# Kernel tuning notes

Measured on AMD Instinct MI355X. Metric: run time of the kernel, lower is better.

The kernel has to match this reference:

```python
import jax, jax.numpy as jnp
import numpy as np

SRC_LEN, TGT_LEN, BATCH = 256, 128, 256
NH, NE, NSYM = 512, 256, 64


def setup_inputs() -> dict:
    key = jax.random.key(0)
    ks = jax.random.split(key, 14)
    w = lambda k, shape: jax.random.normal(k, shape, jnp.float32) * 0.05
    return {
        "src_enc": jax.random.normal(ks[0], (SRC_LEN, BATCH, NH), jnp.float32),
        "tgt": jax.random.randint(ks[1], (TGT_LEN, BATCH, 1), 0, NSYM, jnp.int32),
        "src_lengths": jax.random.randint(ks[2], (BATCH,), 1, SRC_LEN + 1, jnp.int32),
        "emb_table": w(ks[3], (NSYM, NE)),
        "Ws_w": w(ks[4], (NH, NH)), "Ws_b": jnp.zeros((NH,), jnp.float32),
        "Wz_w": w(ks[5], (NH, NE + 2 * NH)), "Wz_b": jnp.zeros((NH,), jnp.float32),
        "Wr_w": w(ks[6], (NH, NE + 2 * NH)), "Wr_b": jnp.zeros((NH,), jnp.float32),
        "Wn_w": w(ks[7], (NH, NE + 2 * NH)), "Wn_b": jnp.zeros((NH,), jnp.float32),
        "Wa_w": w(ks[8], (NH, 2 * NH)), "Wa_b": jnp.zeros((NH,), jnp.float32),
        "va_w": w(ks[9], (1, NH)),
        "Wo_w": w(ks[10], (NH, NE + 2 * NH)), "Wo_b": jnp.zeros((NH,), jnp.float32),
    }


def reference(src_enc, tgt, src_lengths, emb_table,
              Ws_w, Ws_b, Wz_w, Wz_b, Wr_w, Wr_b, Wn_w, Wn_b,
              Wa_w, Wa_b, va_w, Wo_w, Wo_b):
    src_len, batch, nh = src_enc.shape
    # src_mask: [src_len, batch] True where position < length
    mask = jnp.arange(src_len)[:, None] < src_lengths[None, :]
    tgt_embed = emb_table[tgt[..., 0]]                     # [T, B, E]
    s0 = jnp.tanh(src_enc[0] @ Ws_w.T + Ws_b)              # [B, H]
    # Split Wa into the s-part and src_enc-part; encoder projection is
    # loop-invariant, compute it once (same math as cat+Linear).
    Wa_s, Wa_e = Wa_w[:, :nh], Wa_w[:, nh:]
    enc_proj = jnp.einsum('sbh,gh->sbg', src_enc, Wa_e) + Wa_b  # [S, B, H]
    va = va_w[0]                                           # [H]
    neg_inf = jnp.float32(-jnp.inf)

    def step(s, emb_i):
        h = jnp.tanh(enc_proj + s @ Wa_s.T)                # [S, B, H]
        ei = jnp.einsum('sbh,h->sb', h, va)                # [S, B]
        ei = jnp.where(mask, ei, neg_inf)
        ai = jax.nn.softmax(ei, axis=0)                    # [S, B]
        ci = jnp.einsum('sb,sbh->bh', ai, src_enc)         # [B, H]
        x = jnp.concatenate([emb_i, s, ci], axis=-1)       # [B, E+2H]
        ti = x @ Wo_w.T + Wo_b
        zi = jax.nn.sigmoid(x @ Wz_w.T + Wz_b)
        ri = jax.nn.sigmoid(x @ Wr_w.T + Wr_b)
        xn = jnp.concatenate([emb_i, ri * s, ci], axis=-1)
        ni = jnp.tanh(xn @ Wn_w.T + Wn_b)
        s_new = (1.0 - zi) * s + zi * ni
        return s_new, (ti, s, ai.T)

    _, (dec_outputs, dec_states, dec_attns) = jax.lax.scan(step, s0, tgt_embed[:-1])
    # dec_outputs/dec_states: [T-1, B, H]; dec_attns: [T-1, B, S]
    return dec_outputs, dec_states, dec_attns
```

## Files before the change

kernel.cpp:

```cpp
#include <hip/hip_runtime.h>
#include <hip/hip_bf16.h>
#include <cstdint>
#include <cstddef>

namespace {

constexpr int S_LEN  = 256;
constexpr int BATCH  = 256;
constexpr int NH     = 512;
constexpr int NE     = 256;
constexpr int NSTEPS = 127;
constexpr int KX     = NE + 2*NH;
constexpr int N1     = 3*NH;
constexpr size_t SB        = (size_t)S_LEN * BATCH;
constexpr size_t SRC_ELEMS = SB * NH;

typedef __attribute__((ext_vector_type(8))) short  short8v;
typedef __attribute__((ext_vector_type(4))) float  float4v;

__device__ __forceinline__ float bf2f(unsigned short u) {
  union { unsigned int i; float f; } c; c.i = ((unsigned int)u) << 16; return c.f;
}
__device__ __forceinline__ unsigned short f2bf(float f) {
  union { float f; unsigned int i; } c; c.f = f;
  unsigned int x = c.i;
  return (unsigned short)((x + 0x7FFFu + ((x >> 16) & 1u)) >> 16);
}
__device__ __forceinline__ float fast_tanh(float x) {
  float ax = __builtin_fabsf(x);
  float e  = __expf(-2.f * ax);
  float r  = (1.f - e) * __builtin_amdgcn_rcpf(1.f + e);
  return x < 0.f ? -r : r;
}
__device__ __forceinline__ float fast_sigmoid(float x) {
  return __builtin_amdgcn_rcpf(1.f + __expf(-x));
}


__global__ void k_conv_src(const float* __restrict__ src, unsigned short* __restrict__ dst) {
  size_t i = (size_t)blockIdx.x * blockDim.x + threadIdx.x;
  size_t stride = (size_t)gridDim.x * blockDim.x;
  for (size_t j = i * 4; j < SRC_ELEMS; j += stride * 4) {
    float4 v = *(const float4*)(src + j);
    dst[j+0] = f2bf(v.x); dst[j+1] = f2bf(v.y);
    dst[j+2] = f2bf(v.z); dst[j+3] = f2bf(v.w);
  }
}

__global__ void k_conv_w(const float* __restrict__ Wo, const float* __restrict__ Wz,
                         const float* __restrict__ Wr, const float* __restrict__ Wn,
                         const float* __restrict__ Wa,
                         const float* __restrict__ Wob, const float* __restrict__ Wzb,
                         const float* __restrict__ Wrb,
                         unsigned short* __restrict__ W1, unsigned short* __restrict__ WnB,
                         unsigned short* __restrict__ Was, unsigned short* __restrict__ Wae,
                         float* __restrict__ b1) {
  const int TOT_W1 = N1 * KX;
  const int TOT_WN = NH * KX;
  const int TOT_WA = NH * NH;
  const int total  = TOT_W1 + TOT_WN + 2*TOT_WA + N1;
  int i = blockIdx.x * blockDim.x + threadIdx.x;
  int stride = gridDim.x * blockDim.x;
  for (; i < total; i += stride) {
    int idx = i;
    if (idx < TOT_W1) {
      int row = idx / KX, col = idx % KX;
      float v = (row < NH) ? Wo[row*KX+col]
              : (row < 2*NH) ? Wz[(row-NH)*KX+col]
                             : Wr[(row-2*NH)*KX+col];
      W1[idx] = f2bf(v);
    } else if ((idx -= TOT_W1) < TOT_WN) {
      WnB[idx] = f2bf(Wn[idx]);
    } else if ((idx -= TOT_WN) < TOT_WA) {
      int g = idx / NH, j = idx % NH;
      Was[idx] = f2bf(Wa[g*(2*NH) + j]);
    } else if ((idx -= TOT_WA) < TOT_WA) {
      int g = idx / NH, h = idx % NH;
      Wae[idx] = f2bf(Wa[g*(2*NH) + NH + h]);
    } else {
      idx -= TOT_WA;
      b1[idx] = (idx < NH) ? Wob[idx] : (idx < 2*NH) ? Wzb[idx-NH] : Wrb[idx-2*NH];
    }
  }
}

__global__ void k_emb(const int* __restrict__ tgt, const float* __restrict__ table,
                      unsigned short* __restrict__ emb) {
  const int total = NSTEPS * BATCH * NE;
  int i = blockIdx.x * blockDim.x + threadIdx.x;
  int stride = gridDim.x * blockDim.x;
  for (; i < total; i += stride) {
    int e  = i & (NE - 1);
    int tb = i >> 8;
    int sym = tgt[tb];
    emb[i] = f2bf(table[sym * NE + e]);
  }
}

__global__ __launch_bounds__(256) void k_s0(
    const float* __restrict__ src, const float* __restrict__ Wsw,
    const float* __restrict__ Wsb, const unsigned short* __restrict__ emb0,
    float* __restrict__ s_f32, unsigned short* __restrict__ x) {
  __shared__ float sv[NH];
  const int b = blockIdx.x, tid = threadIdx.x;
  sv[tid]       = src[(size_t)b*NH + tid];
  sv[tid + 256] = src[(size_t)b*NH + tid + 256];
  __syncthreads();
  for (int j = tid; j < NH; j += 256) {
    float acc = Wsb[j];
    const float* wr = Wsw + (size_t)j*NH;
    #pragma unroll 8
    for (int h = 0; h < NH; h++) acc += sv[h] * wr[h];
    float s = fast_tanh(acc);
    s_f32[b*NH + j]     = s;
    x[b*KX + NE + j]    = f2bf(s);
  }
  if (tid < NE) x[b*KX + tid] = emb0[b*NE + tid];
}

template<bool OUT_BF16, bool HAS_BIAS>
__global__ __launch_bounds__(256) void k_gemm(
    const unsigned short* __restrict__ A, int lda,
    const unsigned short* __restrict__ B, int ldb,
    void* __restrict__ C, int ldc,
    const float* __restrict__ bias, int K) {
  __shared__ alignas(16) unsigned short As[64][32];
  __shared__ alignas(16) unsigned short Bs[64][32];
  const int tid  = threadIdx.x;
  const int m0   = blockIdx.x * 64, n0 = blockIdx.y * 64;
  const int lane = tid & 63, wave = tid >> 6;
  const int wm   = (wave >> 1) * 32, wn = (wave & 1) * 32;
  const int srow = tid >> 2, scol = (tid & 3) * 8;
  const int fr   = lane & 15, kq = lane >> 4;
  float4v acc00 = {0.f,0.f,0.f,0.f}, acc01 = {0.f,0.f,0.f,0.f};
  float4v acc10 = {0.f,0.f,0.f,0.f}, acc11 = {0.f,0.f,0.f,0.f};
  const unsigned short* Aptr = A + (size_t)(m0 + srow) * lda + scol;
  const unsigned short* Bptr = B + (size_t)(n0 + srow) * ldb + scol;
  for (int k0 = 0; k0 < K; k0 += 32) {
    *(short8v*)&As[srow][scol] = *(const short8v*)(Aptr + k0);
    *(short8v*)&Bs[srow][scol] = *(const short8v*)(Bptr + k0);
    __syncthreads();
    short8v a0 = *(const short8v*)&As[wm + fr][kq*8];
    short8v a1 = *(const short8v*)&As[wm + 16 + fr][kq*8];
    short8v b0 = *(const short8v*)&Bs[wn + fr][kq*8];
    short8v b1 = *(const short8v*)&Bs[wn + 16 + fr][kq*8];
    acc00 = __builtin_amdgcn_mfma_f32_16x16x32_bf16(a0, b0, acc00, 0, 0, 0);
    acc01 = __builtin_amdgcn_mfma_f32_16x16x32_bf16(a0, b1, acc01, 0, 0, 0);
    acc10 = __builtin_amdgcn_mfma_f32_16x16x32_bf16(a1, b0, acc10, 0, 0, 0);
    acc11 = __builtin_amdgcn_mfma_f32_16x16x32_bf16(a1, b1, acc11, 0, 0, 0);
    __syncthreads();
  }
  const int rq = lane >> 4;
  #pragma unroll
  for (int am = 0; am < 2; am++) {
    float4v accb0 = am ? acc10 : acc00;
    float4v accb1 = am ? acc11 : acc01;
    #pragma unroll
    for (int r = 0; r < 4; r++) {
      int row = m0 + wm + am*16 + rq*4 + r;
      int c0  = n0 + wn + fr;
      int c1  = n0 + wn + 16 + fr;
      float v0 = accb0[r], v1 = accb1[r];
      if (HAS_BIAS) { v0 += bias[c0]; v1 += bias[c1]; }
      if (OUT_BF16) {
        ((unsigned short*)C)[(size_t)row*ldc + c0] = f2bf(v0);
        ((unsigned short*)C)[(size_t)row*ldc + c1] = f2bf(v1);
      } else {
        ((float*)C)[(size_t)row*ldc + c0] = v0;
        ((float*)C)[(size_t)row*ldc + c1] = v1;
      }
    }
  }
}

__global__ __launch_bounds__(512) void k_attn(
    const unsigned short* __restrict__ ep,
    const unsigned short* __restrict__ srcb,
    const float* __restrict__ sWa,
    const float* __restrict__ va,
    const int* __restrict__ slen,
    float* __restrict__ attn_out,
    unsigned short* __restrict__ x) {
  __shared__ float q[NH];
  __shared__ float vas[NH];
  __shared__ float ei[S_LEN];
  __shared__ float ai[S_LEN];
  __shared__ float red[8];
  const int b = blockIdx.x, tid = threadIdx.x;
  const int lane = tid & 63, wave = tid >> 6;
  q[tid]   = sWa[b*NH + tid];
  vas[tid] = va[tid];
  __syncthreads();
  const int len = slen[b];

  for (int s = wave; s < S_LEN; s += 8) {
    const unsigned short* p = ep + ((size_t)s*BATCH + b)*NH + lane*8;
    short8v v = *(const short8v*)p;
    float acc = 0.f;
    const int g0 = lane*8;
    #pragma unroll
    for (int j = 0; j < 8; j++) {
      float hv = fast_tanh(bf2f((unsigned short)v[j]) + q[g0+j]);
      acc += hv * vas[g0+j];
    }
    #pragma unroll
    for (int off = 32; off > 0; off >>= 1) acc += __shfl_xor(acc, off, 64);
    if (lane == 0) ei[s] = (s < len) ? acc : -3.0e38f;
  }
  __syncthreads();

  float e = (tid < S_LEN) ? ei[tid] : -3.0e38f;
  float m = e;
  #pragma unroll
  for (int off = 32; off > 0; off >>= 1) m = fmaxf(m, __shfl_xor(m, off, 64));
  if (lane == 0) red[wave] = m;
  __syncthreads();
  m = red[0];
  #pragma unroll
  for (int w = 1; w < 8; w++) m = fmaxf(m, red[w]);
  float p = (tid < S_LEN) ? __expf(e - m) : 0.f;
  float sum = p;
  #pragma unroll
  for (int off = 32; off > 0; off >>= 1) sum += __shfl_xor(sum, off, 64);
  __syncthreads();
  if (lane == 0) red[wave] = sum;
  __syncthreads();
  float tot = red[0];
  #pragma unroll
  for (int w = 1; w < 8; w++) tot += red[w];
  float inv = __builtin_amdgcn_rcpf(tot);
  if (tid < S_LEN) {
    float a = p * inv;
    ai[tid] = a;
    attn_out[(size_t)b*S_LEN + tid] = a;
  }
  __syncthreads();

  float acc = 0.f;
  const unsigned short* sp = srcb + (size_t)b*NH + tid;
  #pragma unroll 8
  for (int s = 0; s < S_LEN; s++) acc += ai[s] * bf2f(sp[(size_t)s * BATCH * NH]);
  x[b*KX + NE + NH + tid] = f2bf(acc);
}

__global__ __launch_bounds__(512) void k_mid(
    const float* __restrict__ Y, const float* __restrict__ s_f32,
    float* __restrict__ dec_out_t, float* __restrict__ zi,
    unsigned short* __restrict__ x) {
  const int b = blockIdx.x, tid = threadIdx.x;
  dec_out_t[(size_t)b*NH + tid] = Y[(size_t)b*N1 + tid];
  zi[b*NH + tid] = fast_sigmoid(Y[(size_t)b*N1 + NH + tid]);
  float r = fast_sigmoid(Y[(size_t)b*N1 + 2*NH + tid]);
  x[b*KX + NE + tid] = f2bf(r * s_f32[b*NH + tid]);
}

__global__ __launch_bounds__(512) void k_final(
    const float* __restrict__ npre, const float* __restrict__ zi,
    float* __restrict__ s_f32, float* __restrict__ dec_states_t,
    unsigned short* __restrict__ x, const unsigned short* __restrict__ emb_next,
    int has_next) {
  const int b = blockIdx.x, tid = threadIdx.x;
  float n  = fast_tanh(npre[b*NH + tid]);
  float z  = zi[b*NH + tid];
  float so = s_f32[b*NH + tid];
  float sn = (1.f - z)*so + z*n;
  dec_states_t[(size_t)b*NH + tid] = so;
  s_f32[b*NH + tid]  = sn;
  x[b*KX + NE + tid] = f2bf(sn);
  if (has_next && tid < NE) x[b*KX + tid] = emb_next[b*NE + tid];
}

}

extern "C" void kernel_launch(void* const* d_in, const int* in_sizes, int n_in,
                              void* d_out, int out_size, void* d_ws, size_t ws_size,
                              hipStream_t stream) {
  const float* src_enc  = (const float*)d_in[0];
  const int*   tgt      = (const int*)d_in[1];
  const int*   slen     = (const int*)d_in[2];
  const float* emb_tab  = (const float*)d_in[3];
  const float* Wsw      = (const float*)d_in[4];
  const float* Wsb      = (const float*)d_in[5];
  const float* Wzw      = (const float*)d_in[6];
  const float* Wzb      = (const float*)d_in[7];
  const float* Wrw      = (const float*)d_in[8];
  const float* Wrb      = (const float*)d_in[9];
  const float* Wnw      = (const float*)d_in[10];
  const float* Wnb      = (const float*)d_in[11];
  const float* Waw      = (const float*)d_in[12];
  const float* Wab      = (const float*)d_in[13];
  const float* vaw      = (const float*)d_in[14];
  const float* Wow      = (const float*)d_in[15];
  const float* Wob      = (const float*)d_in[16];

  char* ws = (char*)d_ws;
  size_t off = 0;
  auto alloc = [&](size_t bytes) -> void* {
    void* p = ws + off;
    off = (off + bytes + 255) & ~(size_t)255;
    return p;
  };
  unsigned short* src_bf = (unsigned short*)alloc(SRC_ELEMS * 2);
  unsigned short* ep     = (unsigned short*)alloc(SRC_ELEMS * 2);
  unsigned short* emb_bf = (unsigned short*)alloc((size_t)NSTEPS*BATCH*NE*2);
  unsigned short* W1     = (unsigned short*)alloc((size_t)N1*KX*2);
  unsigned short* WnB    = (unsigned short*)alloc((size_t)NH*KX*2);
  unsigned short* Was    = (unsigned short*)alloc((size_t)NH*NH*2);
  unsigned short* Wae    = (unsigned short*)alloc((size_t)NH*NH*2);
  float*          b1     = (float*)alloc((size_t)N1*4);
  unsigned short* x      = (unsigned short*)alloc((size_t)BATCH*KX*2);
  float*          s_f32  = (float*)alloc((size_t)BATCH*NH*4);
  float*          sWa    = (float*)alloc((size_t)BATCH*NH*4);
  float*          Y      = (float*)alloc((size_t)BATCH*N1*4);
  float*          zi     = (float*)alloc((size_t)BATCH*NH*4);
  float*          npre   = (float*)alloc((size_t)BATCH*NH*4);

  float* out         = (float*)d_out;
  float* dec_outputs = out;
  float* dec_states  = out + (size_t)NSTEPS*BATCH*NH;
  float* dec_attns   = dec_states + (size_t)NSTEPS*BATCH*NH;

  k_conv_src<<<4096, 256, 0, stream>>>(src_enc, src_bf);
  k_conv_w<<<2048, 256, 0, stream>>>(Wow, Wzw, Wrw, Wnw, Waw, Wob, Wzb, Wrb,
                                     W1, WnB, Was, Wae, b1);
  k_emb<<<2048, 256, 0, stream>>>(tgt, emb_tab, emb_bf);
  k_s0<<<BATCH, 256, 0, stream>>>(src_enc, Wsw, Wsb, emb_bf, s_f32, x);
  k_gemm<true, true><<<dim3(SB/64, NH/64), 256, 0, stream>>>(
      src_bf, NH, Wae, NH, ep, NH, Wab, NH);

  for (int t = 0; t < NSTEPS; t++) {
    k_gemm<false, false><<<dim3(BATCH/64, NH/64), 256, 0, stream>>>(
        x + NE, KX, Was, NH, sWa, NH, nullptr, NH);
    k_attn<<<BATCH, 512, 0, stream>>>(ep, src_bf, sWa, vaw, slen,
                                      dec_attns + (size_t)t*BATCH*S_LEN, x);
    k_gemm<false, true><<<dim3(BATCH/64, N1/64), 256, 0, stream>>>(
        x, KX, W1, KX, Y, N1, b1, KX);
    k_mid<<<BATCH, 512, 0, stream>>>(Y, s_f32, dec_outputs + (size_t)t*BATCH*NH, zi, x);
    k_gemm<false, true><<<dim3(BATCH/64, NH/64), 256, 0, stream>>>(
        x, KX, WnB, KX, npre, NH, Wnb, KX);
    k_final<<<BATCH, 512, 0, stream>>>(npre, zi, s_f32,
                                       dec_states + (size_t)t*BATCH*NH, x,
                                       emb_bf + (size_t)(t+1)*BATCH*NE,
                                       (t+1) < NSTEPS ? 1 : 0);
  }
}
```

Before: 11.83 ms.

## Fuse GRU gate elementwise ops into GEMM epilogues and split Wn by input part

Splits the Wn projection so the emb and ci terms are computed together with the Wo/Wz/Wr GEMM (N=2048), and only the r*s part needs a second small K=512 GEMM. The k_mid and k_final elementwise kernels are folded into GEMM epilogues, and the concatenated x buffer is replaced by separate pointers read directly by the GEMM. The GEMM moves to 64-wide K tiles with double-buffered, XOR-swizzled LDS, and the s0 projection now uses the MFMA GEMM. This cuts launches and intermediate traffic per step and shrinks the Wn GEMM's K, at the cost of branchy epilogues and more A-load pointer logic.

```diff
diff --git a/kernel.cpp b/kernel.cpp
--- a/kernel.cpp
+++ b/kernel.cpp
@@ -10,34 +10,33 @@
 constexpr int NH     = 512;
 constexpr int NE     = 256;
 constexpr int NSTEPS = 127;
-constexpr int KX     = NE + 2*NH;
-constexpr int N1     = 3*NH;
+constexpr int N1     = 2048;
 constexpr size_t SB        = (size_t)S_LEN * BATCH;
 constexpr size_t SRC_ELEMS = SB * NH;
 
 typedef __attribute__((ext_vector_type(8))) short  short8v;
 typedef __attribute__((ext_vector_type(4))) float  float4v;
-
-__device__ __forceinline__ float bf2f(unsigned short u) {
+typedef unsigned short us;
+
+constexpr int EPI_F32 = 0, EPI_EPROJ = 1, EPI_STEP1 = 2, EPI_STEP2 = 3, EPI_S0 = 4;
+
+__device__ __forceinline__ float bf2f(us u) {
   union { unsigned int i; float f; } c; c.i = ((unsigned int)u) << 16; return c.f;
 }
-__device__ __forceinline__ unsigned short f2bf(float f) {
+__device__ __forceinline__ us f2bf(float f) {
   union { float f; unsigned int i; } c; c.f = f;
   unsigned int x = c.i;
-  return (unsigned short)((x + 0x7FFFu + ((x >> 16) & 1u)) >> 16);
-}
-__device__ __forceinline__ float fast_tanh(float x) {
-  float ax = __builtin_fabsf(x);
-  float e  = __expf(-2.f * ax);
-  float r  = (1.f - e) * __builtin_amdgcn_rcpf(1.f + e);
-  return x < 0.f ? -r : r;
-}
-__device__ __forceinline__ float fast_sigmoid(float x) {
+  return (us)((x + 0x7FFFu + ((x >> 16) & 1u)) >> 16);
+}
+__device__ __forceinline__ float tanh2(float x) {
+  return 1.f - 2.f * __builtin_amdgcn_rcpf(__expf(2.f * x) + 1.f);
+}
+__device__ __forceinline__ float sigm(float x) {
   return __builtin_amdgcn_rcpf(1.f + __expf(-x));
 }
 
 
-__global__ void k_conv_src(const float* __restrict__ src, unsigned short* __restrict__ dst) {
+__global__ void k_conv_src(const float* __restrict__ src, us* __restrict__ dst) {
   size_t i = (size_t)blockIdx.x * blockDim.x + threadIdx.x;
   size_t stride = (size_t)gridDim.x * blockDim.x;
   for (size_t j = i * 4; j < SRC_ELEMS; j += stride * 4) {
@@ -49,43 +48,53 @@
 
 __global__ void k_conv_w(const float* __restrict__ Wo, const float* __restrict__ Wz,
                          const float* __restrict__ Wr, const float* __restrict__ Wn,
-                         const float* __restrict__ Wa,
+                         const float* __restrict__ Wa, const float* __restrict__ Ws,
                          const float* __restrict__ Wob, const float* __restrict__ Wzb,
-                         const float* __restrict__ Wrb,
-                         unsigned short* __restrict__ W1, unsigned short* __restrict__ WnB,
-                         unsigned short* __restrict__ Was, unsigned short* __restrict__ Wae,
-                         float* __restrict__ b1) {
-  const int TOT_W1 = N1 * KX;
-  const int TOT_WN = NH * KX;
-  const int TOT_WA = NH * NH;
-  const int total  = TOT_W1 + TOT_WN + 2*TOT_WA + N1;
+                         const float* __restrict__ Wrb, const float* __restrict__ Wnb,
+                         us* __restrict__ W1cat, us* __restrict__ Wns,
+                         us* __restrict__ Was, us* __restrict__ Wae,
+                         us* __restrict__ Wsbf, float* __restrict__ bcat) {
+  const int T1 = 2048 * 1280;
+  const int T2 = 512 * 512;
+  const int total = T1 + 4 * T2 + 2048;
   int i = blockIdx.x * blockDim.x + threadIdx.x;
   int stride = gridDim.x * blockDim.x;
   for (; i < total; i += stride) {
     int idx = i;
-    if (idx < TOT_W1) {
-      int row = idx / KX, col = idx % KX;
-      float v = (row < NH) ? Wo[row*KX+col]
-              : (row < 2*NH) ? Wz[(row-NH)*KX+col]
-                             : Wr[(row-2*NH)*KX+col];
-      W1[idx] = f2bf(v);
-    } else if ((idx -= TOT_W1) < TOT_WN) {
-      WnB[idx] = f2bf(Wn[idx]);
-    } else if ((idx -= TOT_WN) < TOT_WA) {
-      int g = idx / NH, j = idx % NH;
-      Was[idx] = f2bf(Wa[g*(2*NH) + j]);
-    } else if ((idx -= TOT_WA) < TOT_WA) {
-      int g = idx / NH, h = idx % NH;
-      Wae[idx] = f2bf(Wa[g*(2*NH) + NH + h]);
+    if (idx < T1) {
+      int row = idx / 1280, col = idx - row * 1280;
+      float v;
+      if      (row < 512)  v = Wo[row * 1280 + col];
+      else if (row < 1024) v = Wz[(row - 512) * 1280 + col];
+      else if (row < 1536) v = Wr[(row - 1024) * 1280 + col];
+      else {
+        int g = row - 1536;
+        v = (col >= 256 && col < 768) ? 0.f : Wn[g * 1280 + col];
+      }
+      W1cat[idx] = f2bf(v);
+    } else if ((idx -= T1) < T2) {
+      int g = idx >> 9, j = idx & 511;
+      Wns[idx] = f2bf(Wn[g * 1280 + 256 + j]);
+    } else if ((idx -= T2) < T2) {
+      int g = idx >> 9, h = idx & 511;
+      Was[idx] = f2bf(Wa[g * 1024 + h]);
+    } else if ((idx -= T2) < T2) {
+      int g = idx >> 9, h = idx & 511;
+      Wae[idx] = f2bf(Wa[g * 1024 + 512 + h]);
+    } else if ((idx -= T2) < T2) {
+      Wsbf[idx] = f2bf(Ws[idx]);
     } else {
-      idx -= TOT_WA;
-      b1[idx] = (idx < NH) ? Wob[idx] : (idx < 2*NH) ? Wzb[idx-NH] : Wrb[idx-2*NH];
+      idx -= T2;
+      bcat[idx] = (idx < 512) ? Wob[idx]
+                : (idx < 1024) ? Wzb[idx - 512]
+                : (idx < 1536) ? Wrb[idx - 1024]
+                               : Wnb[idx - 1536];
     }
   }
 }
 
 __global__ void k_emb(const int* __restrict__ tgt, const float* __restrict__ table,
-                      unsigned short* __restrict__ emb) {
+                      us* __restrict__ emb) {
   const int total = NSTEPS * BATCH * NE;
   int i = blockIdx.x * blockDim.x + threadIdx.x;
   int stride = gridDim.x * blockDim.x;
@@ -97,112 +106,156 @@
   }
 }
 
-__global__ __launch_bounds__(256) void k_s0(
-    const float* __restrict__ src, const float* __restrict__ Wsw,
-    const float* __restrict__ Wsb, const unsigned short* __restrict__ emb0,
-    float* __restrict__ s_f32, unsigned short* __restrict__ x) {
-  __shared__ float sv[NH];
-  const int b = blockIdx.x, tid = threadIdx.x;
-  sv[tid]       = src[(size_t)b*NH + tid];
-  sv[tid + 256] = src[(size_t)b*NH + tid + 256];
-  __syncthreads();
-  for (int j = tid; j < NH; j += 256) {
-    float acc = Wsb[j];
-    const float* wr = Wsw + (size_t)j*NH;
-    #pragma unroll 8
-    for (int h = 0; h < NH; h++) acc += sv[h] * wr[h];
-    float s = fast_tanh(acc);
-    s_f32[b*NH + j]     = s;
-    x[b*KX + NE + j]    = f2bf(s);
-  }
-  if (tid < NE) x[b*KX + tid] = emb0[b*NE + tid];
-}
-
-template<bool OUT_BF16, bool HAS_BIAS>
-__global__ __launch_bounds__(256) void k_gemm(
-    const unsigned short* __restrict__ A, int lda,
-    const unsigned short* __restrict__ B, int ldb,
-    void* __restrict__ C, int ldc,
-    const float* __restrict__ bias, int K) {
-  __shared__ alignas(16) unsigned short As[64][32];
-  __shared__ alignas(16) unsigned short Bs[64][32];
-  const int tid  = threadIdx.x;
-  const int m0   = blockIdx.x * 64, n0 = blockIdx.y * 64;
+template<int EPI>
+__global__ __launch_bounds__(256) void k_g64(
+    const us* __restrict__ A0, const us* __restrict__ A1, const us* __restrict__ A2,
+    const us* __restrict__ Bw, int K,
+    const float* __restrict__ bias,
+    float* __restrict__ f0, float* __restrict__ f1, float* __restrict__ f2,
+    us* __restrict__ g0,
+    const float* __restrict__ sf) {
+  constexpr bool X3 = (EPI == EPI_STEP1);
+  __shared__ us As[2][4096];
+  __shared__ us Bs[2][4096];
+  const int tid = threadIdx.x;
+  const int m0 = blockIdx.x * 64, n0 = blockIdx.y * 64;
+  const int srow  = tid >> 2;
+  const int c0    = (tid & 3) * 16;
+  const int cbyte = c0 * 2;
+  const int nit   = K >> 6;
+  short8v ar0, ar1, br0, br1;
+
+  auto loadA = [&](int k0) {
+    const int cc0 = k0 + c0, cc1 = cc0 + 8;
+    if (X3) {
+      const us* p0 = (cc0 < 256) ? A0 + (size_t)(m0 + srow) * 256 + cc0
+                   : (cc0 < 768) ? A1 + (size_t)(m0 + srow) * 512 + (cc0 - 256)
+                                 : A2 + (size_t)(m0 + srow) * 512 + (cc0 - 768);
+      const us* p1 = (cc1 < 256) ? A0 + (size_t)(m0 + srow) * 256 + cc1
+                   : (cc1 < 768) ? A1 + (size_t)(m0 + srow) * 512 + (cc1 - 256)
+                                 : A2 + (size_t)(m0 + srow) * 512 + (cc1 - 768);
+      ar0 = *(const short8v*)p0;
+      ar1 = *(const short8v*)p1;
+    } else {
+      const us* p = A0 + (size_t)(m0 + srow) * K + cc0;
+      ar0 = *(const short8v*)p;
+      ar1 = *(const short8v*)(p + 8);
+    }
+    const us* q = Bw + (size_t)(n0 + srow) * K + cc0;
+    br0 = *(const short8v*)q;
+    br1 = *(const short8v*)(q + 8);
+  };
+  auto stage = [&](int buf) {
+    char* ab = (char*)As + buf * 8192;
+    char* bb = (char*)Bs + buf * 8192;
+    const int sw = (srow & 7) << 4;
+    const int o0 = srow * 128 + (cbyte ^ sw);
+    const int o1 = srow * 128 + ((cbyte + 16) ^ sw);
+    *(short8v*)(ab + o0) = ar0;
+    *(short8v*)(ab + o1) = ar1;
+    *(short8v*)(bb + o0) = br0;
+    *(short8v*)(bb + o1) = br1;
+  };
+
   const int lane = tid & 63, wave = tid >> 6;
-  const int wm   = (wave >> 1) * 32, wn = (wave & 1) * 32;
-  const int srow = tid >> 2, scol = (tid & 3) * 8;
-  const int fr   = lane & 15, kq = lane >> 4;
-  float4v acc00 = {0.f,0.f,0.f,0.f}, acc01 = {0.f,0.f,0.f,0.f};
-  float4v acc10 = {0.f,0.f,0.f,0.f}, acc11 = {0.f,0.f,0.f,0.f};
-  const unsigned short* Aptr = A + (size_t)(m0 + srow) * lda + scol;
-  const unsigned short* Bptr = B + (size_t)(n0 + srow) * ldb + scol;
-  for (int k0 = 0; k0 < K; k0 += 32) {
-    *(short8v*)&As[srow][scol] = *(const short8v*)(Aptr + k0);
-    *(short8v*)&Bs[srow][scol] = *(const short8v*)(Bptr + k0);
+  const int wm = (wave >> 1) * 32, wn = (wave & 1) * 32;
+  const int fr = lane & 15, kq = lane >> 4;
+  const int ra0 = wm + fr, ra1 = wm + 16 + fr;
+  const int rb0 = wn + fr, rb1 = wn + 16 + fr;
+  float4v acc00 = {0,0,0,0}, acc01 = {0,0,0,0}, acc10 = {0,0,0,0}, acc11 = {0,0,0,0};
+
+  loadA(0);
+  stage(0);
+  for (int it = 0; it < nit; ++it) {
     __syncthreads();
-    short8v a0 = *(const short8v*)&As[wm + fr][kq*8];
-    short8v a1 = *(const short8v*)&As[wm + 16 + fr][kq*8];
-    short8v b0 = *(const short8v*)&Bs[wn + fr][kq*8];
-    short8v b1 = *(const short8v*)&Bs[wn + 16 + fr][kq*8];
-    acc00 = __builtin_amdgcn_mfma_f32_16x16x32_bf16(a0, b0, acc00, 0, 0, 0);
-    acc01 = __builtin_amdgcn_mfma_f32_16x16x32_bf16(a0, b1, acc01, 0, 0, 0);
-    acc10 = __builtin_amdgcn_mfma_f32_16x16x32_bf16(a1, b0, acc10, 0, 0, 0);
-    acc11 = __builtin_amdgcn_mfma_f32_16x16x32_bf16(a1, b1, acc11, 0, 0, 0);
-    __syncthreads();
-  }
-  const int rq = lane >> 4;
-  #pragma unroll
-  for (int am = 0; am < 2; am++) {
-    float4v accb0 = am ? acc10 : acc00;
-    float4v accb1 = am ? acc11 : acc01;
-    #pragma unroll
-    for (int r = 0; r < 4; r++) {
-      int row = m0 + wm + am*16 + rq*4 + r;
-      int c0  = n0 + wn + fr;
-      int c1  = n0 + wn + 16 + fr;
-      float v0 = accb0[r], v1 = accb1[r];
-      if (HAS_BIAS) { v0 += bias[c0]; v1 += bias[c1]; }
-      if (OUT_BF16) {
-        ((unsigned short*)C)[(size_t)row*ldc + c0] = f2bf(v0);
-        ((unsigned short*)C)[(size_t)row*ldc + c1] = f2bf(v1);
-      } else {
-        ((float*)C)[(size_t)row*ldc + c0] = v0;
-        ((float*)C)[(size_t)row*ldc + c1] = v1;
+    if (it + 1 < nit) loadA((it + 1) << 6);
+    const char* ab = (const char*)As + (it & 1) * 8192;
+    const char* bb = (const char*)Bs + (it & 1) * 8192;
+    #pragma unroll
+    for (int ks = 0; ks < 2; ++ks) {
+      const int cb2 = ks * 64 + kq * 16;
+      short8v a0 = *(const short8v*)(ab + ra0 * 128 + (cb2 ^ ((ra0 & 7) << 4)));
+      short8v a1 = *(const short8v*)(ab + ra1 * 128 + (cb2 ^ ((ra1 & 7) << 4)));
+      short8v b0 = *(const short8v*)(bb + rb0 * 128 + (cb2 ^ ((rb0 & 7) << 4)));
+      short8v b1 = *(const short8v*)(bb + rb1 * 128 + (cb2 ^ ((rb1 & 7) << 4)));
+      acc00 = __builtin_amdgcn_mfma_f32_16x16x32_bf16(a0, b0, acc00, 0, 0, 0);
+      acc01 = __builtin_amdgcn_mfma_f32_16x16x32_bf16(a0, b1, acc01, 0, 0, 0);
+      acc10 = __builtin_amdgcn_mfma_f32_16x16x32_bf16(a1, b0, acc10, 0, 0, 0);
+      acc11 = __builtin_amdgcn_mfma_f32_16x16x32_bf16(a1, b1, acc11, 0, 0, 0);
+    }
+    if (it + 1 < nit) stage((it + 1) & 1);
+  }
+
+  #pragma unroll
+  for (int am = 0; am < 2; ++am) {
+    #pragma unroll
+    for (int bn = 0; bn < 2; ++bn) {
+      float4v a = am ? (bn ? acc11 : acc10) : (bn ? acc01 : acc00);
+      #pragma unroll
+      for (int r = 0; r < 4; ++r) {
+        const int rowO = m0 + wm + am * 16 + kq * 4 + r;
+        const int colO = n0 + wn + bn * 16 + fr;
+        float v = a[r];
+        if (EPI == EPI_F32) {
+          f0[(size_t)rowO * 512 + colO] = v;
+        } else if (EPI == EPI_S0) {
+          float tv = tanh2(v + bias[colO]);
+          f0[(size_t)rowO * 512 + colO] = tv;
+          g0[(size_t)rowO * 512 + colO] = f2bf(tv);
+        } else if (EPI == EPI_EPROJ) {
+          g0[(size_t)rowO * 512 + colO] = f2bf(v + bias[colO]);
+        } else if (EPI == EPI_STEP1) {
+          v += bias[colO];
+          const int q = colO >> 9, j = colO & 511;
+          const size_t idx = (size_t)rowO * 512 + j;
+          if      (q == 0) f0[idx] = v;
+          else if (q == 1) f1[idx] = sigm(v);
+          else if (q == 2) g0[idx] = f2bf(sigm(v) * sf[idx]);
+          else             f2[idx] = v;
+        } else {
+          const size_t idx = (size_t)rowO * 512 + colO;
+          float nv = tanh2(v + f2[idx]);
+          float z  = bias[idx];
+          float so = f1[idx];
+          float sn = (1.f - z) * so + z * nv;
+          f0[idx] = so;
+          f1[idx] = sn;
+          g0[idx] = f2bf(sn);
+        }
       }
     }
   }
 }
 
 __global__ __launch_bounds__(512) void k_attn(
-    const unsigned short* __restrict__ ep,
-    const unsigned short* __restrict__ srcb,
+    const us* __restrict__ ep,
+    const us* __restrict__ srcb,
     const float* __restrict__ sWa,
     const float* __restrict__ va,
     const int* __restrict__ slen,
     float* __restrict__ attn_out,
-    unsigned short* __restrict__ x) {
-  __shared__ float q[NH];
-  __shared__ float vas[NH];
+    us* __restrict__ ci_bf) {
   __shared__ float ei[S_LEN];
   __shared__ float ai[S_LEN];
   __shared__ float red[8];
   const int b = blockIdx.x, tid = threadIdx.x;
   const int lane = tid & 63, wave = tid >> 6;
-  q[tid]   = sWa[b*NH + tid];
-  vas[tid] = va[tid];
-  __syncthreads();
+  const int g0 = lane * 8;
+  float qv[8], vv[8];
+  {
+    const float* qp = sWa + b * NH + g0;
+    const float* vp = va + g0;
+    #pragma unroll
+    for (int j = 0; j < 8; j++) { qv[j] = qp[j]; vv[j] = vp[j]; }
+  }
   const int len = slen[b];
 
   for (int s = wave; s < S_LEN; s += 8) {
-    const unsigned short* p = ep + ((size_t)s*BATCH + b)*NH + lane*8;
-    short8v v = *(const short8v*)p;
+    short8v v = *(const short8v*)(ep + ((size_t)s * BATCH + b) * NH + g0);
     float acc = 0.f;
-    const int g0 = lane*8;
-    #pragma unroll
-    for (int j = 0; j < 8; j++) {
-      float hv = fast_tanh(bf2f((unsigned short)v[j]) + q[g0+j]);
-      acc += hv * vas[g0+j];
-    }
+    #pragma unroll
+    for (int j = 0; j < 8; j++)
+      acc += tanh2(bf2f((us)v[j]) + qv[j]) * vv[j];
     #pragma unroll
     for (int off = 32; off > 0; off >>= 1) acc += __shfl_xor(acc, off, 64);
     if (lane == 0) ei[s] = (s < len) ? acc : -3.0e38f;
@@ -232,42 +285,15 @@
   if (tid < S_LEN) {
     float a = p * inv;
     ai[tid] = a;
-    attn_out[(size_t)b*S_LEN + tid] = a;
+    attn_out[(size_t)b * S_LEN + tid] = a;
   }
   __syncthreads();
 
   float acc = 0.f;
-  const unsigned short* sp = srcb + (size_t)b*NH + tid;
+  const us* sp = srcb + (size_t)b * NH + tid;
   #pragma unroll 8
   for (int s = 0; s < S_LEN; s++) acc += ai[s] * bf2f(sp[(size_t)s * BATCH * NH]);
-  x[b*KX + NE + NH + tid] = f2bf(acc);
-}
-
-__global__ __launch_bounds__(512) void k_mid(
-    const float* __restrict__ Y, const float* __restrict__ s_f32,
-    float* __restrict__ dec_out_t, float* __restrict__ zi,
-    unsigned short* __restrict__ x) {
-  const int b = blockIdx.x, tid = threadIdx.x;
-  dec_out_t[(size_t)b*NH + tid] = Y[(size_t)b*N1 + tid];
-  zi[b*NH + tid] = fast_sigmoid(Y[(size_t)b*N1 + NH + tid]);
-  float r = fast_sigmoid(Y[(size_t)b*N1 + 2*NH + tid]);
-  x[b*KX + NE + tid] = f2bf(r * s_f32[b*NH + tid]);
-}
-
-__global__ __launch_bounds__(512) void k_final(
-    const float* __restrict__ npre, const float* __restrict__ zi,
-    float* __restrict__ s_f32, float* __restrict__ dec_states_t,
-    unsigned short* __restrict__ x, const unsigned short* __restrict__ emb_next,
-    int has_next) {
-  const int b = blockIdx.x, tid = threadIdx.x;
-  float n  = fast_tanh(npre[b*NH + tid]);
-  float z  = zi[b*NH + tid];
-  float so = s_f32[b*NH + tid];
-  float sn = (1.f - z)*so + z*n;
-  dec_states_t[(size_t)b*NH + tid] = so;
-  s_f32[b*NH + tid]  = sn;
-  x[b*KX + NE + tid] = f2bf(sn);
-  if (has_next && tid < NE) x[b*KX + tid] = emb_next[b*NE + tid];
+  ci_bf[b * NH + tid] = f2bf(acc);
 }
 
 }
@@ -300,47 +326,48 @@
     off = (off + bytes + 255) & ~(size_t)255;
     return p;
   };
-  unsigned short* src_bf = (unsigned short*)alloc(SRC_ELEMS * 2);
-  unsigned short* ep     = (unsigned short*)alloc(SRC_ELEMS * 2);
-  unsigned short* emb_bf = (unsigned short*)alloc((size_t)NSTEPS*BATCH*NE*2);
-  unsigned short* W1     = (unsigned short*)alloc((size_t)N1*KX*2);
-  unsigned short* WnB    = (unsigned short*)alloc((size_t)NH*KX*2);
-  unsigned short* Was    = (unsigned short*)alloc((size_t)NH*NH*2);
-  unsigned short* Wae    = (unsigned short*)alloc((size_t)NH*NH*2);
-  float*          b1     = (float*)alloc((size_t)N1*4);
-  unsigned short* x      = (unsigned short*)alloc((size_t)BATCH*KX*2);
-  float*          s_f32  = (float*)alloc((size_t)BATCH*NH*4);
-  float*          sWa    = (float*)alloc((size_t)BATCH*NH*4);
-  float*          Y      = (float*)alloc((size_t)BATCH*N1*4);
-  float*          zi     = (float*)alloc((size_t)BATCH*NH*4);
-  float*          npre   = (float*)alloc((size_t)BATCH*NH*4);
+  us*    src_bf = (us*)alloc(SRC_ELEMS * 2);
+  us*    ep     = (us*)alloc(SRC_ELEMS * 2);
+  us*    emb_bf = (us*)alloc((size_t)NSTEPS * BATCH * NE * 2);
+  us*    W1cat  = (us*)alloc((size_t)N1 * 1280 * 2);
+  us*    Wns    = (us*)alloc((size_t)512 * 512 * 2);
+  us*    Was    = (us*)alloc((size_t)512 * 512 * 2);
+  us*    Wae    = (us*)alloc((size_t)512 * 512 * 2);
+  us*    Wsbf   = (us*)alloc((size_t)512 * 512 * 2);
+  float* bcat   = (float*)alloc((size_t)N1 * 4);
+  float* s_f32  = (float*)alloc((size_t)BATCH * NH * 4);
+  us*    s_bf   = (us*)alloc((size_t)BATCH * NH * 2);
+  float* sWa    = (float*)alloc((size_t)BATCH * NH * 4);
+  float* zi     = (float*)alloc((size_t)BATCH * NH * 4);
+  float* npart  = (float*)alloc((size_t)BATCH * NH * 4);
+  us*    xn_bf  = (us*)alloc((size_t)BATCH * NH * 2);
+  us*    ci_bf  = (us*)alloc((size_t)BATCH * NH * 2);
 
   float* out         = (float*)d_out;
   float* dec_outputs = out;
-  float* dec_states  = out + (size_t)NSTEPS*BATCH*NH;
-  float* dec_attns   = dec_states + (size_t)NSTEPS*BATCH*NH;
+  float* dec_states  = out + (size_t)NSTEPS * BATCH * NH;
+  float* dec_attns   = dec_states + (size_t)NSTEPS * BATCH * NH;
 
   k_conv_src<<<4096, 256, 0, stream>>>(src_enc, src_bf);
-  k_conv_w<<<2048, 256, 0, stream>>>(Wow, Wzw, Wrw, Wnw, Waw, Wob, Wzb, Wrb,
-                                     W1, WnB, Was, Wae, b1);
+  k_conv_w<<<2048, 256, 0, stream>>>(Wow, Wzw, Wrw, Wnw, Waw, Wsw,
+                                     Wob, Wzb, Wrb, Wnb,
+                                     W1cat, Wns, Was, Wae, Wsbf, bcat);
   k_emb<<<2048, 256, 0, stream>>>(tgt, emb_tab, emb_bf);
-  k_s0<<<BATCH, 256, 0, stream>>>(src_enc, Wsw, Wsb, emb_bf, s_f32, x);
-  k_gemm<true, true><<<dim3(SB/64, NH/64), 256, 0, stream>>>(
-      src_bf, NH, Wae, NH, ep, NH, Wab, NH);
+  k_g64<EPI_S0><<<dim3(4, 8), 256, 0, stream>>>(
+      src_bf, nullptr, nullptr, Wsbf, 512, Wsb, s_f32, nullptr, nullptr, s_bf, nullptr);
+  k_g64<EPI_EPROJ><<<dim3(1024, 8), 256, 0, stream>>>(
+      src_bf, nullptr, nullptr, Wae, 512, Wab, nullptr, nullptr, nullptr, ep, nullptr);
 
   for (int t = 0; t < NSTEPS; t++) {
-    k_gemm<false, false><<<dim3(BATCH/64, NH/64), 256, 0, stream>>>(
-        x + NE, KX, Was, NH, sWa, NH, nullptr, NH);
+    k_g64<EPI_F32><<<dim3(4, 8), 256, 0, stream>>>(
+        s_bf, nullptr, nullptr, Was, 512, nullptr, sWa, nullptr, nullptr, nullptr, nullptr);
     k_attn<<<BATCH, 512, 0, stream>>>(ep, src_bf, sWa, vaw, slen,
-                                      dec_attns + (size_t)t*BATCH*S_LEN, x);
-    k_gemm<false, true><<<dim3(BATCH/64, N1/64), 256, 0, stream>>>(
-        x, KX, W1, KX, Y, N1, b1, KX);
-    k_mid<<<BATCH, 512, 0, stream>>>(Y, s_f32, dec_outputs + (size_t)t*BATCH*NH, zi, x);
-    k_gemm<false, true><<<dim3(BATCH/64, NH/64), 256, 0, stream>>>(
-        x, KX, WnB, KX, npre, NH, Wnb, KX);
-    k_final<<<BATCH, 512, 0, stream>>>(npre, zi, s_f32,
-                                       dec_states + (size_t)t*BATCH*NH, x,
-                                       emb_bf + (size_t)(t+1)*BATCH*NE,
-                                       (t+1) < NSTEPS ? 1 : 0);
-  }
-}
+                                      dec_attns + (size_t)t * BATCH * S_LEN, ci_bf);
+    k_g64<EPI_STEP1><<<dim3(4, 32), 256, 0, stream>>>(
+        emb_bf + (size_t)t * BATCH * NE, s_bf, ci_bf, W1cat, 1280, bcat,
+        dec_outputs + (size_t)t * BATCH * NH, zi, npart, xn_bf, s_f32);
+    k_g64<EPI_STEP2><<<dim3(4, 8), 256, 0, stream>>>(
+        xn_bf, nullptr, nullptr, Wns, 512, zi,
+        dec_states + (size_t)t * BATCH * NH, s_f32, npart, s_bf, nullptr);
+  }
+}
```

New measurement: 9.611 ms. 1.23x faster.
